# Kernel optimization log

Hardware: AMD Instinct MI355X
Metric: run time of the kernel (lower is better)

Reference implementation:

```python
import jax, jax.numpy as jnp
import numpy as np

EPS = 1e-5   # torch BatchNorm2d default eps
HEADS = 4


def conv1x1_bn(x, w, g, b, m, v):
    # 1x1 conv (no bias) == channel matmul, then inference-mode BatchNorm
    y = jnp.einsum('oc,bchw->bohw', w, x)
    s = g / jnp.sqrt(v + EPS)
    return y * s[None, :, None, None] + (b - m * s)[None, :, None, None]


def dwconv3x3_bn(x, w, g, b, m, v):
    # depthwise 3x3 conv, padding 1 (autopad), groups=C, then BatchNorm
    C = x.shape[1]
    y = jax.lax.conv_general_dilated(
        x, w, window_strides=(1, 1), padding=((1, 1), (1, 1)),
        dimension_numbers=('NCHW', 'OIHW', 'NCHW'), feature_group_count=C)
    s = g / jnp.sqrt(v + EPS)
    return y * s[None, :, None, None] + (b - m * s)[None, :, None, None]


def split_heads(x):
    b, c, h, w = x.shape
    hd = c // HEADS
    return x.reshape(b, HEADS, hd, h * w).transpose(0, 1, 3, 2)  # [b,heads,n,hd]


def merge_heads(x, h, w):
    b, heads, n, hd = x.shape
    return x.transpose(0, 1, 3, 2).reshape(b, heads * hd, h, w)


def setup_inputs() -> dict:
    key = jax.random.key(0)
    B, C, H, W = 4, 256, 48, 48
    ks = jax.random.split(key, 32)
    inp = {
        'q': jax.random.normal(ks[0], (B, C, H, W), jnp.float32),
        'k': jax.random.normal(ks[1], (B, C, H, W), jnp.float32),
        'v': jax.random.normal(ks[2], (B, C, H, W), jnp.float32),
    }
    i = 3
    for name in ['wq', 'wk', 'wv', 'proj']:
        inp[name + '_w'] = jax.random.normal(ks[i], (C, C), jnp.float32) * 0.02; i += 1
    inp['pe_w'] = jax.random.normal(ks[i], (C, 1, 3, 3), jnp.float32) * 0.1; i += 1
    for name in ['wq', 'wk', 'wv', 'pe', 'proj']:
        inp[name + '_g'] = jax.random.uniform(ks[i], (C,), jnp.float32, 0.5, 1.5); i += 1
        inp[name + '_b'] = jax.random.normal(ks[i], (C,), jnp.float32) * 0.1; i += 1
        inp[name + '_m'] = jax.random.normal(ks[i], (C,), jnp.float32) * 0.1; i += 1
        inp[name + '_v'] = jax.random.uniform(ks[i], (C,), jnp.float32, 0.5, 1.5); i += 1
    return inp


def reference(q, k, v,
              wq_w, wk_w, wv_w, proj_w, pe_w,
              wq_g, wq_b, wq_m, wq_v,
              wk_g, wk_b, wk_m, wk_v,
              wv_g, wv_b, wv_m, wv_v,
              pe_g, pe_b, pe_m, pe_v,
              proj_g, proj_b, proj_m, proj_v):
    H, W = q.shape[2], q.shape[3]
    qf = conv1x1_bn(q, wq_w, wq_g, wq_b, wq_m, wq_v)
    kf = conv1x1_bn(k, wk_w, wk_g, wk_b, wk_m, wk_v)
    vf = conv1x1_bn(v, wv_w, wv_g, wv_b, wv_m, wv_v)
    qh = split_heads(qf)  # [b,heads,n,hd]
    kh = split_heads(kf)
    vh = split_heads(vf)
    scale = qh.shape[-1] ** -0.5
    attn = jax.nn.softmax(jnp.einsum('bhnd,bhmd->bhnm', qh, kh) * scale, axis=-1)
    y = jnp.einsum('bhnm,bhmd->bhnd', attn, vh)
    y = merge_heads(y, H, W) + dwconv3x3_bn(merge_heads(qh, H, W), pe_w, pe_g, pe_b, pe_m, pe_v)
    return conv1x1_bn(y, proj_w, proj_g, proj_b, proj_m, proj_v)
```

## Files before the change

kernel.cpp:

```cpp
#include <hip/hip_runtime.h>
#include <math.h>

#define HEADS 4
#define HD    64
#define CCH   256
#define NB    4
#define HH    48
#define WW    48
#define NN    (HH*WW)
#define EPSBN 1e-5f
#define KSCL  0.18033688f
#define BCN   (NB*CCH*NN)
#define NSP   4

typedef unsigned short ushort_t;
typedef __attribute__((ext_vector_type(8))) short bfrag;
typedef __attribute__((ext_vector_type(4))) float f32x4;
typedef __attribute__((ext_vector_type(16))) float f32x16;

#define MFMA   __builtin_amdgcn_mfma_f32_16x16x32_bf16
#define MFMA32 __builtin_amdgcn_mfma_f32_32x32x16_bf16

static __device__ __forceinline__ ushort_t f2bf(float x) {
    unsigned int u = __float_as_uint(x);
    unsigned int r = (u + 0x7fffu + ((u >> 16) & 1u)) >> 16;
    return (ushort_t)r;
}
static __device__ __forceinline__ unsigned cvtpk(float lo, float hi) {
    unsigned r;
    asm("v_cvt_pk_bf16_f32 %0, %1, %2" : "=v"(r) : "v"(lo), "v"(hi));
    return r;
}
static __device__ __forceinline__ float fexp2(float x) {
    float r;
    asm("v_exp_f32 %0, %1" : "=v"(r) : "v"(x));
    return r;
}
static __device__ __forceinline__ float bflo(unsigned u) { return __uint_as_float(u << 16); }
static __device__ __forceinline__ float bfhi(unsigned u) { return __uint_as_float(u & 0xffff0000u); }

static __device__ __forceinline__ void gload16(const void* g, void* l) {
    __builtin_amdgcn_global_load_lds(
        (const __attribute__((address_space(1))) void*)g,
        (__attribute__((address_space(3))) void*)l, 16, 0, 0);
}

struct PrepWP {
    const float* W[4];
    const float* G[4]; const float* Bb[4]; const float* Mm[4]; const float* Vv[4];
    const float* pew; const float* peg; const float* peb; const float* pem; const float* pev;
    ushort_t* W4; float* bias4; ushort_t* pw2; float* pbias;
};
__global__ __launch_bounds__(256)
void prep_w(PrepWP P)
{
    const int blk = blockIdx.x, tid = threadIdx.x;
    if (blk == 128) {
        int c = tid;
        float s = P.peg[c] * rsqrtf(P.pev[c] + EPSBN);
        for (int tap = 0; tap < 9; ++tap)
            P.pw2[tap * CCH + c] = f2bf(P.pew[c * 9 + tap] * s);
        P.pbias[c] = P.peb[c] - P.pem[c] * s;
        return;
    }
    int g  = blk * 256 + tid;
    int cv = g >> 13;
    int o  = (g >> 5) & 255;
    int c8 = g & 31;
    float s  = P.G[cv][o] * rsqrtf(P.Vv[cv][o] + EPSBN);
    float s2 = (cv == 1) ? s * KSCL : s;
    const float* w = P.W[cv] + (size_t)o * CCH + c8 * 8;
    uint4 u;
    u.x = cvtpk(w[0]*s2, w[1]*s2); u.y = cvtpk(w[2]*s2, w[3]*s2);
    u.z = cvtpk(w[4]*s2, w[5]*s2); u.w = cvtpk(w[6]*s2, w[7]*s2);
    *(uint4*)&P.W4[((size_t)cv * CCH + o) * CCH + c8 * 8] = u;
    if (c8 == 0) {
        float bb = (P.Bb[cv][o] - P.Mm[cv][o] * s);
        P.bias4[cv * CCH + o] = (cv == 1) ? bb * KSCL : bb;
    }
}

template<int PROJ>
__global__ __launch_bounds__(512)
void conv_gemm(const float* __restrict__ qf, const float* __restrict__ kf,
               const float* __restrict__ vf, const ushort_t* __restrict__ T,
               const ushort_t* __restrict__ W4, const float* __restrict__ bias4,
               ushort_t* __restrict__ qnd, ushort_t* __restrict__ knd,
               ushort_t* __restrict__ vcn, float* __restrict__ outf)
{
    __shared__ ushort_t Ts[64][264];
    __shared__ ushort_t Ws[64][264];
    const int nt = blockIdx.x, ot = blockIdx.y, z = blockIdx.z;
    const int which = PROJ ? 3 : (z >> 2);
    const int b = z & 3;
    const int tid = threadIdx.x;
    const int n0 = nt * 64, o0 = ot * 64;
    const ushort_t* Wsrc = W4 + (size_t)which * CCH * CCH + (size_t)o0 * CCH;
    const float*    bias = bias4 + which * CCH;

    if (!PROJ) {
#pragma unroll
        for (int i = 0; i < 4; ++i) {
            int idx = tid + i * 512;
            int r = idx >> 5, c16 = idx & 31;
            *(uint4*)&Ws[r][c16 * 8] = *(const uint4*)&Wsrc[(size_t)r * CCH + c16 * 8];
        }
        const float* Xf = (which == 0) ? qf : (which == 1) ? kf : vf;
        const float* Xb = Xf + (size_t)b * CCH * NN + n0;
        const int n = tid & 63;
#pragma unroll
        for (int p = 0; p < 4; ++p) {
            int c0 = (tid >> 6) * 8 + p * 64;
            const float* src = Xb + (size_t)c0 * NN + n;
            float vv[8];
#pragma unroll
            for (int j = 0; j < 8; ++j) vv[j] = src[(size_t)j * NN];
            uint4 u;
            u.x = cvtpk(vv[0], vv[1]); u.y = cvtpk(vv[2], vv[3]);
            u.z = cvtpk(vv[4], vv[5]); u.w = cvtpk(vv[6], vv[7]);
            *(uint4*)&Ts[n][c0] = u;
        }
    } else {
        const ushort_t* Tsrc = T + ((size_t)b * NN + n0) * CCH;
#pragma unroll
        for (int i = 0; i < 4; ++i) {
            int idx = tid + i * 512;
            int r = idx >> 5, c16 = idx & 31;
            *(uint4*)&Ts[r][c16 * 8] = *(const uint4*)&Tsrc[(size_t)r * CCH + c16 * 8];
            *(uint4*)&Ws[r][c16 * 8] = *(const uint4*)&Wsrc[(size_t)r * CCH + c16 * 8];
        }
    }
    __syncthreads();
    const int wv = tid >> 6, lane = tid & 63, lr = lane & 15, lg = lane >> 4;
    const int qn = (wv >> 1) * 16, qo = (wv & 1) * 32;
    f32x4 acc[2];
    acc[0] = (f32x4){0.f, 0.f, 0.f, 0.f};
    acc[1] = (f32x4){0.f, 0.f, 0.f, 0.f};

    if (!PROJ && (z >> 2) < 2) {
#pragma unroll
        for (int k8 = 0; k8 < 8; ++k8) {
            const int kc = k8 * 32 + lg * 8;
            bfrag ta  = *(const bfrag*)&Ts[qn + lr][kc];
            bfrag wa0 = *(const bfrag*)&Ws[qo + lr][kc];
            bfrag wa1 = *(const bfrag*)&Ws[qo + 16 + lr][kc];
            acc[0] = MFMA(ta, wa0, acc[0], 0, 0, 0);
            acc[1] = MFMA(ta, wa1, acc[1], 0, 0, 0);
        }
    } else {
#pragma unroll
        for (int k8 = 0; k8 < 8; ++k8) {
            const int kc = k8 * 32 + lg * 8;
            bfrag ta  = *(const bfrag*)&Ts[qn + lr][kc];
            bfrag wa0 = *(const bfrag*)&Ws[qo + lr][kc];
            bfrag wa1 = *(const bfrag*)&Ws[qo + 16 + lr][kc];
            acc[0] = MFMA(wa0, ta, acc[0], 0, 0, 0);
            acc[1] = MFMA(wa1, ta, acc[1], 0, 0, 0);
        }
    }

    __syncthreads();
    if (!PROJ && which < 2) {
        ushort_t (*Ot)[72] = (ushort_t(*)[72])Ts;
        float bv[2] = { bias[o0 + qo + lr], bias[o0 + qo + 16 + lr] };
#pragma unroll
        for (int j = 0; j < 2; ++j)
#pragma unroll
            for (int r = 0; r < 4; ++r)
                Ot[qn + lg * 4 + r][qo + j * 16 + lr] = f2bf(acc[j][r] + bv[j]);
        __syncthreads();
        ushort_t* out = (which == 0) ? qnd : knd;
        {
            int r = tid >> 3, sg = tid & 7;
            *(uint4*)&out[(((size_t)b * HEADS + ot) * NN + n0 + r) * HD + sg * 8] =
                *(const uint4*)&Ot[r][sg * 8];
        }
    } else if (!PROJ) {
        ushort_t (*Ot)[72] = (ushort_t(*)[72])Ts;
#pragma unroll
        for (int j = 0; j < 2; ++j)
#pragma unroll
            for (int r = 0; r < 4; ++r) {
                float bv = bias[o0 + qo + j * 16 + lg * 4 + r];
                Ot[qo + j * 16 + lg * 4 + r][qn + lr] = f2bf(acc[j][r] + bv);
            }
        __syncthreads();
        {
            int r = tid >> 3, sg = tid & 7;
            *(uint4*)&vcn[((size_t)b * CCH + o0 + r) * NN + n0 + sg * 8] =
                *(const uint4*)&Ot[r][sg * 8];
        }
    } else {
        float (*Of)[68] = (float(*)[68])Ts;
#pragma unroll
        for (int j = 0; j < 2; ++j)
#pragma unroll
            for (int r = 0; r < 4; ++r) {
                float bv = bias[o0 + qo + j * 16 + lg * 4 + r];
                Of[qo + j * 16 + lg * 4 + r][qn + lr] = acc[j][r] + bv;
            }
        __syncthreads();
#pragma unroll
        for (int i = 0; i < 2; ++i) {
            int idx = tid + i * 512;
            int r = idx >> 4, c4 = idx & 15;
            *(float4*)&outf[((size_t)b * CCH + o0 + r) * NN + n0 + c4 * 4] =
                *(const float4*)&Of[r][c4 * 4];
        }
    }
}

__global__ __launch_bounds__(256, 4)
void attn_kernel(const ushort_t* __restrict__ Qnd,
                 const ushort_t* __restrict__ Knd,
                 const ushort_t* __restrict__ Vcn,
                 ushort_t* __restrict__ Op,
                 float* __restrict__ Larr)
{
    __shared__ __align__(16) char smem[32768];

    const int tid = threadIdx.x;
    const int lin0 = blockIdx.x + 18 * blockIdx.y + 288 * blockIdx.z;
    const int w    = (lin0 & 7) * 144 + (lin0 >> 3);
    const int qt = w % 18;
    const int bh = (w / 18) & 15;
    const int sp = w / 288;
    const int b = bh >> 2, h = bh & 3;
    const int lane = tid & 63, wv = tid >> 6;
    const int l31 = lane & 31, hi = lane >> 5, l7 = lane & 7;
    const int lrow = lane >> 3, lslot = (lane & 7) ^ lrow;
    const int n0 = qt * 128;
    const size_t ndb = (size_t)(b * HEADS + h) * NN * HD;
    const size_t cnb = ((size_t)b * CCH + h * HD) * NN;

    const char* kgp = (const char*)(Knd + ndb) + (size_t)(sp * 576 + wv * 16 + lrow) * 128 + lslot * 16;
    const char* vgp = (const char*)(Vcn + cnb + sp * 576) + (size_t)(wv * 16 + lrow) * (NN * 2) + lslot * 16;
    char* kls = smem + wv * 2048;
    char* vls = smem + 16384 + wv * 2048;

#define STAGE(buf, t) do { \
    const char* kp_ = kgp + (size_t)(t) * 8192; \
    const char* vp_ = vgp + (size_t)(t) * 128; \
    char* kd_ = kls + (buf) * 8192; \
    char* vd_ = vls + (buf) * 8192; \
    gload16(kp_,              kd_); \
    gload16(kp_ + 1024,       kd_ + 1024); \
    gload16(vp_,              vd_); \
    gload16(vp_ + 8 * (NN*2), vd_ + 1024); \
} while (0)

    bfrag qb[4];
    {
        const ushort_t* qbase = Qnd + ndb + (size_t)(n0 + wv * 32 + l31) * HD + hi * 8;
#pragma unroll
        for (int ds = 0; ds < 4; ++ds)
            qb[ds] = *(const bfrag*)&qbase[ds * 16];
    }

    f32x16 o[2];
#pragma unroll
    for (int db = 0; db < 2; ++db)
#pragma unroll
        for (int j = 0; j < 16; ++j) o[db][j] = 0.f;
    float lacc0 = 0.f, lacc1 = 0.f;

    STAGE(0, 0);

    for (int t = 0; t < 9; ++t) {
        const int cur = t & 1;
        asm volatile("s_waitcnt vmcnt(0)" ::: "memory");
        __builtin_amdgcn_s_barrier();
        if (t < 8) STAGE(cur ^ 1, t + 1);
        const char* Kb = smem + cur * 8192;
        const char* Vb = smem + 16384 + cur * 8192;

        bfrag pf[4];
#pragma unroll
        for (int kb = 0; kb < 2; ++kb) {
            f32x16 s;
#pragma unroll
            for (int j = 0; j < 16; ++j) s[j] = 0.f;
            __builtin_amdgcn_s_setprio(1);
#pragma unroll
            for (int ds = 0; ds < 4; ++ds) {
                const char* ka_p = Kb + (kb * 32 + l31) * 128 + (((2 * ds + hi) ^ l7) << 4);
                bfrag ka = *(const bfrag*)ka_p;
                s = MFMA32(ka, qb[ds], s, 0, 0, 0);
            }
            __builtin_amdgcn_s_setprio(0);
            float e[16];
#pragma unroll
            for (int j = 0; j < 16; ++j) e[j] = fexp2(s[j]);
#pragma unroll
            for (int j = 0; j < 8; ++j) { lacc0 += e[2 * j]; lacc1 += e[2 * j + 1]; }
            unsigned u[4][2];
#pragma unroll
            for (int g = 0; g < 4; ++g) {
                u[g][0] = cvtpk(e[4 * g + 0], e[4 * g + 1]);
                u[g][1] = cvtpk(e[4 * g + 2], e[4 * g + 3]);
            }
#pragma unroll
            for (int ks = 0; ks < 2; ++ks) {
                asm("v_permlane32_swap_b32 %0, %1" : "+v"(u[2*ks][0]), "+v"(u[2*ks+1][0]));
                asm("v_permlane32_swap_b32 %0, %1" : "+v"(u[2*ks][1]), "+v"(u[2*ks+1][1]));
                uint4 fw = { u[2*ks][0], u[2*ks][1], u[2*ks+1][0], u[2*ks+1][1] };
                pf[kb * 2 + ks] = *(const bfrag*)&fw;
            }
        }

        __builtin_amdgcn_s_setprio(1);
#pragma unroll
        for (int db = 0; db < 2; ++db)
#pragma unroll
            for (int ks = 0; ks < 4; ++ks) {
                const char* va_p = Vb + (db * 32 + l31) * 128 + (((2 * ks + hi) ^ l7) << 4);
                bfrag va = *(const bfrag*)va_p;
                o[db] = MFMA32(va, pf[ks], o[db], 0, 0, 0);
            }
        __builtin_amdgcn_s_setprio(0);
    }
#undef STAGE
    __builtin_amdgcn_s_barrier();

    float lacc = lacc0 + lacc1;
    lacc += __shfl_xor(lacc, 32);
    if (hi == 0)
        Larr[(size_t)(sp * 16 + bh) * NN + n0 + wv * 32 + l31] = lacc;

    unsigned (*Osb)[36] = (unsigned(*)[36])smem;
    {
        int row = wv * 32 + l31;
#pragma unroll
        for (int db = 0; db < 2; ++db)
#pragma unroll
            for (int g = 0; g < 4; ++g) {
                uint2 pk;
                pk.x = cvtpk(o[db][4 * g + 0], o[db][4 * g + 1]);
                pk.y = cvtpk(o[db][4 * g + 2], o[db][4 * g + 3]);
                *(uint2*)&Osb[row][16 * db + 4 * g + 2 * hi] = pk;
            }
    }
    __syncthreads();
    ushort_t* opb = Op + (size_t)sp * BCN + ((size_t)b * NN + n0) * CCH + h * HD;
    for (int idx = tid; idx < 1024; idx += 256) {
        int n = idx >> 3, s4 = idx & 7;
        *(uint4*)&opb[(size_t)n * CCH + s4 * 8] = *(const uint4*)&Osb[n][s4 * 4];
    }
}

__global__ __launch_bounds__(256)
void fuse_kernel(const ushort_t* __restrict__ Op, const float* __restrict__ Larr,
                 const ushort_t* __restrict__ Qnd,
                 const ushort_t* __restrict__ pw2, const float* __restrict__ pbias,
                 ushort_t* __restrict__ yt)
{
    const int tid = threadIdx.x;
    const int b  = blockIdx.x / 288;
    const int n0 = (blockIdx.x % 288) * 8;
    const int c8 = tid & 31, ns = tid >> 5;
    const int n  = n0 + ns;
    const int h  = c8 >> 3, c0 = c8 * 8;

    const ushort_t* o0p = Op + ((size_t)b * NN + n) * CCH + c0;
    float acc[8] = {0.f, 0.f, 0.f, 0.f, 0.f, 0.f, 0.f, 0.f};
#pragma unroll
    for (int s = 0; s < NSP; ++s) {
        uint4 u = *(const uint4*)&o0p[(size_t)s * BCN];
        acc[0] += bflo(u.x); acc[1] += bfhi(u.x);
        acc[2] += bflo(u.y); acc[3] += bfhi(u.y);
        acc[4] += bflo(u.z); acc[5] += bfhi(u.z);
        acc[6] += bflo(u.w); acc[7] += bfhi(u.w);
    }
    int mi = (b * HEADS + h) * NN + n;
    float ls = 0.f;
#pragma unroll
    for (int s = 0; s < NSP; ++s) ls += Larr[(size_t)s * 16 * NN + mi];
    float rinv = 1.0f / ls;
#pragma unroll
    for (int j = 0; j < 8; ++j) acc[j] *= rinv;

    const int x = n % WW, y = n / WW;
    const ushort_t* qb = Qnd + (size_t)(b * HEADS + h) * NN * HD + (c8 & 7) * 8;
#pragma unroll
    for (int ky = 0; ky < 3; ++ky) {
        int yy = y + ky - 1;
        if (yy < 0 || yy >= HH) continue;
#pragma unroll
        for (int kx = 0; kx < 3; ++kx) {
            int xx = x + kx - 1;
            if (xx < 0 || xx >= WW) continue;
            int np = yy * WW + xx;
            uint4 qv = *(const uint4*)&qb[(size_t)np * HD];
            uint4 w4 = *(const uint4*)&pw2[(ky * 3 + kx) * CCH + c0];
            acc[0] += bflo(qv.x) * bflo(w4.x); acc[1] += bfhi(qv.x) * bfhi(w4.x);
            acc[2] += bflo(qv.y) * bflo(w4.y); acc[3] += bfhi(qv.y) * bfhi(w4.y);
            acc[4] += bflo(qv.z) * bflo(w4.z); acc[5] += bfhi(qv.z) * bfhi(w4.z);
            acc[6] += bflo(qv.w) * bflo(w4.w); acc[7] += bfhi(qv.w) * bfhi(w4.w);
        }
    }
    float4 p0 = *(const float4*)&pbias[c0];
    float4 p1 = *(const float4*)&pbias[c0 + 4];
    acc[0] += p0.x; acc[1] += p0.y; acc[2] += p0.z; acc[3] += p0.w;
    acc[4] += p1.x; acc[5] += p1.y; acc[6] += p1.z; acc[7] += p1.w;
    uint4 u;
    u.x = cvtpk(acc[0], acc[1]); u.y = cvtpk(acc[2], acc[3]);
    u.z = cvtpk(acc[4], acc[5]); u.w = cvtpk(acc[6], acc[7]);
    *(uint4*)&yt[((size_t)b * NN + n) * CCH + c0] = u;
}

extern "C" void kernel_launch(void* const* d_in, const int* in_sizes, int n_in,
                              void* d_out, int out_size, void* d_ws, size_t ws_size,
                              hipStream_t stream) {
    const float* q = (const float*)d_in[0];
    const float* k = (const float*)d_in[1];
    const float* v = (const float*)d_in[2];

    char* ws = (char*)d_ws;
    ushort_t* qnd  = (ushort_t*)(ws + 0);
    ushort_t* knd  = (ushort_t*)(ws + 4718592);
    ushort_t* vcn  = (ushort_t*)(ws + 9437184);
    ushort_t* Op   = (ushort_t*)(ws + 14155776);
    ushort_t* yt   = (ushort_t*)(ws + 4718592);
    float*    Larr = (float*)   (ws + 33030144);
    ushort_t* W4   = (ushort_t*)(ws + 33619968);
    float*    bias4= (float*)   (ws + 34144256);
    ushort_t* pw2  = (ushort_t*)(ws + 34148352);
    float*    pbias= (float*)   (ws + 34152960);

    PrepWP P;
    P.W[0] = (const float*)d_in[3]; P.W[1] = (const float*)d_in[4];
    P.W[2] = (const float*)d_in[5]; P.W[3] = (const float*)d_in[6];
    P.G[0]  = (const float*)d_in[8];  P.Bb[0] = (const float*)d_in[9];
    P.Mm[0] = (const float*)d_in[10]; P.Vv[0] = (const float*)d_in[11];
    P.G[1]  = (const float*)d_in[12]; P.Bb[1] = (const float*)d_in[13];
    P.Mm[1] = (const float*)d_in[14]; P.Vv[1] = (const float*)d_in[15];
    P.G[2]  = (const float*)d_in[16]; P.Bb[2] = (const float*)d_in[17];
    P.Mm[2] = (const float*)d_in[18]; P.Vv[2] = (const float*)d_in[19];
    P.G[3]  = (const float*)d_in[24]; P.Bb[3] = (const float*)d_in[25];
    P.Mm[3] = (const float*)d_in[26]; P.Vv[3] = (const float*)d_in[27];
    P.pew = (const float*)d_in[7];
    P.peg = (const float*)d_in[20]; P.peb = (const float*)d_in[21];
    P.pem = (const float*)d_in[22]; P.pev = (const float*)d_in[23];
    P.W4 = W4; P.bias4 = bias4; P.pw2 = pw2; P.pbias = pbias;

    prep_w<<<129, 256, 0, stream>>>(P);

    conv_gemm<0><<<dim3(36, 4, 12), 512, 0, stream>>>(q, k, v, nullptr, W4, bias4,
                                                      qnd, knd, vcn, nullptr);

    attn_kernel<<<dim3(18, 16, NSP), 256, 0, stream>>>(qnd, knd, vcn, Op, Larr);

    fuse_kernel<<<1152, 256, 0, stream>>>(Op, Larr, qnd, pw2, pbias, yt);

    conv_gemm<1><<<dim3(36, 4, 4), 512, 0, stream>>>(nullptr, nullptr, nullptr, yt, W4, bias4,
                                                     nullptr, nullptr, nullptr, (float*)d_out);
}
```

Measured before the change: 75.10 us.

## Fold weight prep into GEMM/fuse kernels and raise attention KV splits to six

```diff
diff --git a/kernel.cpp b/kernel.cpp
--- a/kernel.cpp
+++ b/kernel.cpp
@@ -11,7 +11,6 @@
 #define EPSBN 1e-5f
 #define KSCL  0.18033688f
 #define BCN   (NB*CCH*NN)
-#define NSP   4
 
 typedef unsigned short ushort_t;
 typedef __attribute__((ext_vector_type(8))) short bfrag;
@@ -21,72 +20,42 @@
 #define MFMA   __builtin_amdgcn_mfma_f32_16x16x32_bf16
 #define MFMA32 __builtin_amdgcn_mfma_f32_32x32x16_bf16
 
+static __device__ __forceinline__ unsigned cvtpk(float lo, float hi) {
+    unsigned r;
+    asm("v_cvt_pk_bf16_f32 %0, %1, %2" : "=v"(r) : "v"(lo), "v"(hi));
+    return r;
+}
+static __device__ __forceinline__ float fexp2(float x) {
+    float r;
+    asm("v_exp_f32 %0, %1" : "=v"(r) : "v"(x));
+    return r;
+}
+static __device__ __forceinline__ float bflo(unsigned u) { return __uint_as_float(u << 16); }
+static __device__ __forceinline__ float bfhi(unsigned u) { return __uint_as_float(u & 0xffff0000u); }
+
+static __device__ __forceinline__ void gload16(const void* g, void* l) {
+    __builtin_amdgcn_global_load_lds(
+        (const __attribute__((address_space(1))) void*)g,
+        (__attribute__((address_space(3))) void*)l, 16, 0, 0);
+}
+
 static __device__ __forceinline__ ushort_t f2bf(float x) {
     unsigned int u = __float_as_uint(x);
     unsigned int r = (u + 0x7fffu + ((u >> 16) & 1u)) >> 16;
     return (ushort_t)r;
 }
-static __device__ __forceinline__ unsigned cvtpk(float lo, float hi) {
-    unsigned r;
-    asm("v_cvt_pk_bf16_f32 %0, %1, %2" : "=v"(r) : "v"(lo), "v"(hi));
-    return r;
-}
-static __device__ __forceinline__ float fexp2(float x) {
-    float r;
-    asm("v_exp_f32 %0, %1" : "=v"(r) : "v"(x));
-    return r;
-}
-static __device__ __forceinline__ float bflo(unsigned u) { return __uint_as_float(u << 16); }
-static __device__ __forceinline__ float bfhi(unsigned u) { return __uint_as_float(u & 0xffff0000u); }
-
-static __device__ __forceinline__ void gload16(const void* g, void* l) {
-    __builtin_amdgcn_global_load_lds(
-        (const __attribute__((address_space(1))) void*)g,
-        (__attribute__((address_space(3))) void*)l, 16, 0, 0);
-}
-
-struct PrepWP {
-    const float* W[4];
-    const float* G[4]; const float* Bb[4]; const float* Mm[4]; const float* Vv[4];
-    const float* pew; const float* peg; const float* peb; const float* pem; const float* pev;
-    ushort_t* W4; float* bias4; ushort_t* pw2; float* pbias;
+
+struct ConvP {
+    const float* X0; const float* X1; const float* X2;
+    const ushort_t* T;
+    const float* W[4]; const float* G[4]; const float* Bb[4];
+    const float* Mm[4]; const float* Vv[4];
+    ushort_t* qnd; ushort_t* knd; ushort_t* vcn; float* outf;
 };
-__global__ __launch_bounds__(256)
-void prep_w(PrepWP P)
-{
-    const int blk = blockIdx.x, tid = threadIdx.x;
-    if (blk == 128) {
-        int c = tid;
-        float s = P.peg[c] * rsqrtf(P.pev[c] + EPSBN);
-        for (int tap = 0; tap < 9; ++tap)
-            P.pw2[tap * CCH + c] = f2bf(P.pew[c * 9 + tap] * s);
-        P.pbias[c] = P.peb[c] - P.pem[c] * s;
-        return;
-    }
-    int g  = blk * 256 + tid;
-    int cv = g >> 13;
-    int o  = (g >> 5) & 255;
-    int c8 = g & 31;
-    float s  = P.G[cv][o] * rsqrtf(P.Vv[cv][o] + EPSBN);
-    float s2 = (cv == 1) ? s * KSCL : s;
-    const float* w = P.W[cv] + (size_t)o * CCH + c8 * 8;
-    uint4 u;
-    u.x = cvtpk(w[0]*s2, w[1]*s2); u.y = cvtpk(w[2]*s2, w[3]*s2);
-    u.z = cvtpk(w[4]*s2, w[5]*s2); u.w = cvtpk(w[6]*s2, w[7]*s2);
-    *(uint4*)&P.W4[((size_t)cv * CCH + o) * CCH + c8 * 8] = u;
-    if (c8 == 0) {
-        float bb = (P.Bb[cv][o] - P.Mm[cv][o] * s);
-        P.bias4[cv * CCH + o] = (cv == 1) ? bb * KSCL : bb;
-    }
-}
 
 template<int PROJ>
 __global__ __launch_bounds__(512)
-void conv_gemm(const float* __restrict__ qf, const float* __restrict__ kf,
-               const float* __restrict__ vf, const ushort_t* __restrict__ T,
-               const ushort_t* __restrict__ W4, const float* __restrict__ bias4,
-               ushort_t* __restrict__ qnd, ushort_t* __restrict__ knd,
-               ushort_t* __restrict__ vcn, float* __restrict__ outf)
+void conv_gemm(ConvP P)
 {
     __shared__ ushort_t Ts[64][264];
     __shared__ ushort_t Ws[64][264];
@@ -95,17 +64,29 @@
     const int b = z & 3;
     const int tid = threadIdx.x;
     const int n0 = nt * 64, o0 = ot * 64;
-    const ushort_t* Wsrc = W4 + (size_t)which * CCH * CCH + (size_t)o0 * CCH;
-    const float*    bias = bias4 + which * CCH;
-
+    const float* Wf  = P.W[which];
+    const float* Gf  = P.G[which];
+    const float* Bbf = P.Bb[which];
+    const float* Mmf = P.Mm[which];
+    const float* Vvf = P.Vv[which];
+    const float wmul = (which == 1) ? KSCL : 1.0f;
+
+#pragma unroll
+    for (int i = 0; i < 4; ++i) {
+        int idx = tid + i * 512;
+        int r = idx >> 5, c16 = idx & 31;
+        int o = o0 + r;
+        float s2 = Gf[o] * rsqrtf(Vvf[o] + EPSBN) * wmul;
+        const float* wp = Wf + (size_t)o * CCH + c16 * 8;
+        float4 wa = *(const float4*)&wp[0];
+        float4 wb = *(const float4*)&wp[4];
+        uint4 u;
+        u.x = cvtpk(wa.x * s2, wa.y * s2); u.y = cvtpk(wa.z * s2, wa.w * s2);
+        u.z = cvtpk(wb.x * s2, wb.y * s2); u.w = cvtpk(wb.z * s2, wb.w * s2);
+        *(uint4*)&Ws[r][c16 * 8] = u;
+    }
     if (!PROJ) {
-#pragma unroll
-        for (int i = 0; i < 4; ++i) {
-            int idx = tid + i * 512;
-            int r = idx >> 5, c16 = idx & 31;
-            *(uint4*)&Ws[r][c16 * 8] = *(const uint4*)&Wsrc[(size_t)r * CCH + c16 * 8];
-        }
-        const float* Xf = (which == 0) ? qf : (which == 1) ? kf : vf;
+        const float* Xf = (which == 0) ? P.X0 : (which == 1) ? P.X1 : P.X2;
         const float* Xb = Xf + (size_t)b * CCH * NN + n0;
         const int n = tid & 63;
 #pragma unroll
@@ -121,13 +102,12 @@
             *(uint4*)&Ts[n][c0] = u;
         }
     } else {
-        const ushort_t* Tsrc = T + ((size_t)b * NN + n0) * CCH;
+        const ushort_t* Tsrc = P.T + ((size_t)b * NN + n0) * CCH;
 #pragma unroll
         for (int i = 0; i < 4; ++i) {
             int idx = tid + i * 512;
             int r = idx >> 5, c16 = idx & 31;
             *(uint4*)&Ts[r][c16 * 8] = *(const uint4*)&Tsrc[(size_t)r * CCH + c16 * 8];
-            *(uint4*)&Ws[r][c16 * 8] = *(const uint4*)&Wsrc[(size_t)r * CCH + c16 * 8];
         }
     }
     __syncthreads();
@@ -137,7 +117,7 @@
     acc[0] = (f32x4){0.f, 0.f, 0.f, 0.f};
     acc[1] = (f32x4){0.f, 0.f, 0.f, 0.f};
 
-    if (!PROJ && (z >> 2) < 2) {
+    if (!PROJ && which < 2) {
 #pragma unroll
         for (int k8 = 0; k8 < 8; ++k8) {
             const int kc = k8 * 32 + lg * 8;
@@ -162,14 +142,20 @@
     __syncthreads();
     if (!PROJ && which < 2) {
         ushort_t (*Ot)[72] = (ushort_t(*)[72])Ts;
-        float bv[2] = { bias[o0 + qo + lr], bias[o0 + qo + 16 + lr] };
+        float bv[2];
+#pragma unroll
+        for (int j = 0; j < 2; ++j) {
+            int o = o0 + qo + j * 16 + lr;
+            float s = Gf[o] * rsqrtf(Vvf[o] + EPSBN);
+            bv[j] = (Bbf[o] - Mmf[o] * s) * wmul;
+        }
 #pragma unroll
         for (int j = 0; j < 2; ++j)
 #pragma unroll
             for (int r = 0; r < 4; ++r)
                 Ot[qn + lg * 4 + r][qo + j * 16 + lr] = f2bf(acc[j][r] + bv[j]);
         __syncthreads();
-        ushort_t* out = (which == 0) ? qnd : knd;
+        ushort_t* out = (which == 0) ? P.qnd : P.knd;
         {
             int r = tid >> 3, sg = tid & 7;
             *(uint4*)&out[(((size_t)b * HEADS + ot) * NN + n0 + r) * HD + sg * 8] =
@@ -181,13 +167,15 @@
         for (int j = 0; j < 2; ++j)
 #pragma unroll
             for (int r = 0; r < 4; ++r) {
-                float bv = bias[o0 + qo + j * 16 + lg * 4 + r];
+                int o = o0 + qo + j * 16 + lg * 4 + r;
+                float s = Gf[o] * rsqrtf(Vvf[o] + EPSBN);
+                float bv = Bbf[o] - Mmf[o] * s;
                 Ot[qo + j * 16 + lg * 4 + r][qn + lr] = f2bf(acc[j][r] + bv);
             }
         __syncthreads();
         {
             int r = tid >> 3, sg = tid & 7;
-            *(uint4*)&vcn[((size_t)b * CCH + o0 + r) * NN + n0 + sg * 8] =
+            *(uint4*)&P.vcn[((size_t)b * CCH + o0 + r) * NN + n0 + sg * 8] =
                 *(const uint4*)&Ot[r][sg * 8];
         }
     } else {
@@ -196,7 +184,9 @@
         for (int j = 0; j < 2; ++j)
 #pragma unroll
             for (int r = 0; r < 4; ++r) {
-                float bv = bias[o0 + qo + j * 16 + lg * 4 + r];
+                int o = o0 + qo + j * 16 + lg * 4 + r;
+                float s = Gf[o] * rsqrtf(Vvf[o] + EPSBN);
+                float bv = Bbf[o] - Mmf[o] * s;
                 Of[qo + j * 16 + lg * 4 + r][qn + lr] = acc[j][r] + bv;
             }
         __syncthreads();
@@ -204,12 +194,13 @@
         for (int i = 0; i < 2; ++i) {
             int idx = tid + i * 512;
             int r = idx >> 4, c4 = idx & 15;
-            *(float4*)&outf[((size_t)b * CCH + o0 + r) * NN + n0 + c4 * 4] =
+            *(float4*)&P.outf[((size_t)b * CCH + o0 + r) * NN + n0 + c4 * 4] =
                 *(const float4*)&Of[r][c4 * 4];
         }
     }
 }
 
+template<int NSPT>
 __global__ __launch_bounds__(256, 4)
 void attn_kernel(const ushort_t* __restrict__ Qnd,
                  const ushort_t* __restrict__ Knd,
@@ -217,11 +208,13 @@
                  ushort_t* __restrict__ Op,
                  float* __restrict__ Larr)
 {
+    constexpr int NT    = 36 / NSPT;
+    constexpr int CHUNK = 18 * 16 * NSPT / 8;
     __shared__ __align__(16) char smem[32768];
 
     const int tid = threadIdx.x;
     const int lin0 = blockIdx.x + 18 * blockIdx.y + 288 * blockIdx.z;
-    const int w    = (lin0 & 7) * 144 + (lin0 >> 3);
+    const int w    = (lin0 & 7) * CHUNK + (lin0 >> 3);
     const int qt = w % 18;
     const int bh = (w / 18) & 15;
     const int sp = w / 288;
@@ -233,8 +226,8 @@
     const size_t ndb = (size_t)(b * HEADS + h) * NN * HD;
     const size_t cnb = ((size_t)b * CCH + h * HD) * NN;
 
-    const char* kgp = (const char*)(Knd + ndb) + (size_t)(sp * 576 + wv * 16 + lrow) * 128 + lslot * 16;
-    const char* vgp = (const char*)(Vcn + cnb + sp * 576) + (size_t)(wv * 16 + lrow) * (NN * 2) + lslot * 16;
+    const char* kgp = (const char*)(Knd + ndb) + (size_t)(sp * (NT * 64) + wv * 16 + lrow) * 128 + lslot * 16;
+    const char* vgp = (const char*)(Vcn + cnb + sp * (NT * 64)) + (size_t)(wv * 16 + lrow) * (NN * 2) + lslot * 16;
     char* kls = smem + wv * 2048;
     char* vls = smem + 16384 + wv * 2048;
 
@@ -266,11 +259,11 @@
 
     STAGE(0, 0);
 
-    for (int t = 0; t < 9; ++t) {
+    for (int t = 0; t < NT; ++t) {
         const int cur = t & 1;
         asm volatile("s_waitcnt vmcnt(0)" ::: "memory");
         __builtin_amdgcn_s_barrier();
-        if (t < 8) STAGE(cur ^ 1, t + 1);
+        if (t < NT - 1) STAGE(cur ^ 1, t + 1);
         const char* Kb = smem + cur * 8192;
         const char* Vb = smem + 16384 + cur * 8192;
 
@@ -348,10 +341,13 @@
     }
 }
 
+template<int NSPT>
 __global__ __launch_bounds__(256)
 void fuse_kernel(const ushort_t* __restrict__ Op, const float* __restrict__ Larr,
                  const ushort_t* __restrict__ Qnd,
-                 const ushort_t* __restrict__ pw2, const float* __restrict__ pbias,
+                 const float* __restrict__ pew, const float* __restrict__ peg,
+                 const float* __restrict__ peb, const float* __restrict__ pem,
+                 const float* __restrict__ pev,
                  ushort_t* __restrict__ yt)
 {
     const int tid = threadIdx.x;
@@ -364,7 +360,7 @@
     const ushort_t* o0p = Op + ((size_t)b * NN + n) * CCH + c0;
     float acc[8] = {0.f, 0.f, 0.f, 0.f, 0.f, 0.f, 0.f, 0.f};
 #pragma unroll
-    for (int s = 0; s < NSP; ++s) {
+    for (int s = 0; s < NSPT; ++s) {
         uint4 u = *(const uint4*)&o0p[(size_t)s * BCN];
         acc[0] += bflo(u.x); acc[1] += bfhi(u.x);
         acc[2] += bflo(u.y); acc[3] += bfhi(u.y);
@@ -374,10 +370,19 @@
     int mi = (b * HEADS + h) * NN + n;
     float ls = 0.f;
 #pragma unroll
-    for (int s = 0; s < NSP; ++s) ls += Larr[(size_t)s * 16 * NN + mi];
+    for (int s = 0; s < NSPT; ++s) ls += Larr[(size_t)s * 16 * NN + mi];
     float rinv = 1.0f / ls;
 #pragma unroll
     for (int j = 0; j < 8; ++j) acc[j] *= rinv;
+
+    float ps_[8], pb_[8];
+#pragma unroll
+    for (int j = 0; j < 8; ++j) {
+        int c = c0 + j;
+        float s = peg[c] * rsqrtf(pev[c] + EPSBN);
+        ps_[j] = s;
+        pb_[j] = peb[c] - pem[c] * s;
+    }
 
     const int x = n % WW, y = n / WW;
     const ushort_t* qb = Qnd + (size_t)(b * HEADS + h) * NN * HD + (c8 & 7) * 8;
@@ -391,17 +396,19 @@
             if (xx < 0 || xx >= WW) continue;
             int np = yy * WW + xx;
             uint4 qv = *(const uint4*)&qb[(size_t)np * HD];
-            uint4 w4 = *(const uint4*)&pw2[(ky * 3 + kx) * CCH + c0];
-            acc[0] += bflo(qv.x) * bflo(w4.x); acc[1] += bfhi(qv.x) * bfhi(w4.x);
-            acc[2] += bflo(qv.y) * bflo(w4.y); acc[3] += bfhi(qv.y) * bfhi(w4.y);
-            acc[4] += bflo(qv.z) * bflo(w4.z); acc[5] += bfhi(qv.z) * bfhi(w4.z);
-            acc[6] += bflo(qv.w) * bflo(w4.w); acc[7] += bfhi(qv.w) * bfhi(w4.w);
-        }
-    }
-    float4 p0 = *(const float4*)&pbias[c0];
-    float4 p1 = *(const float4*)&pbias[c0 + 4];
-    acc[0] += p0.x; acc[1] += p0.y; acc[2] += p0.z; acc[3] += p0.w;
-    acc[4] += p1.x; acc[5] += p1.y; acc[6] += p1.z; acc[7] += p1.w;
+            const float* pwc = pew + (size_t)c0 * 9 + (ky * 3 + kx);
+            acc[0] += bflo(qv.x) * (pwc[0]  * ps_[0]);
+            acc[1] += bfhi(qv.x) * (pwc[9]  * ps_[1]);
+            acc[2] += bflo(qv.y) * (pwc[18] * ps_[2]);
+            acc[3] += bfhi(qv.y) * (pwc[27] * ps_[3]);
+            acc[4] += bflo(qv.z) * (pwc[36] * ps_[4]);
+            acc[5] += bfhi(qv.z) * (pwc[45] * ps_[5]);
+            acc[6] += bflo(qv.w) * (pwc[54] * ps_[6]);
+            acc[7] += bfhi(qv.w) * (pwc[63] * ps_[7]);
+        }
+    }
+#pragma unroll
+    for (int j = 0; j < 8; ++j) acc[j] += pb_[j];
     uint4 u;
     u.x = cvtpk(acc[0], acc[1]); u.y = cvtpk(acc[2], acc[3]);
     u.z = cvtpk(acc[4], acc[5]); u.w = cvtpk(acc[6], acc[7]);
@@ -411,23 +418,22 @@
 extern "C" void kernel_launch(void* const* d_in, const int* in_sizes, int n_in,
                               void* d_out, int out_size, void* d_ws, size_t ws_size,
                               hipStream_t stream) {
-    const float* q = (const float*)d_in[0];
-    const float* k = (const float*)d_in[1];
-    const float* v = (const float*)d_in[2];
-
     char* ws = (char*)d_ws;
-    ushort_t* qnd  = (ushort_t*)(ws + 0);
-    ushort_t* knd  = (ushort_t*)(ws + 4718592);
-    ushort_t* vcn  = (ushort_t*)(ws + 9437184);
-    ushort_t* Op   = (ushort_t*)(ws + 14155776);
-    ushort_t* yt   = (ushort_t*)(ws + 4718592);
-    float*    Larr = (float*)   (ws + 33030144);
-    ushort_t* W4   = (ushort_t*)(ws + 33619968);
-    float*    bias4= (float*)   (ws + 34144256);
-    ushort_t* pw2  = (ushort_t*)(ws + 34148352);
-    float*    pbias= (float*)   (ws + 34152960);
-
-    PrepWP P;
+    ushort_t* qnd = (ushort_t*)(ws + 0);
+    ushort_t* knd = (ushort_t*)(ws + 4718592);
+    ushort_t* vcn = (ushort_t*)(ws + 9437184);
+    ushort_t* Op  = (ushort_t*)(ws + 14155776);
+    ushort_t* yt  = (ushort_t*)(ws + 4718592);
+
+    const float* pew = (const float*)d_in[7];
+    const float* peg = (const float*)d_in[20], *peb = (const float*)d_in[21];
+    const float* pem = (const float*)d_in[22], *pev = (const float*)d_in[23];
+
+    ConvP P;
+    P.X0 = (const float*)d_in[0];
+    P.X1 = (const float*)d_in[1];
+    P.X2 = (const float*)d_in[2];
+    P.T  = yt;
     P.W[0] = (const float*)d_in[3]; P.W[1] = (const float*)d_in[4];
     P.W[2] = (const float*)d_in[5]; P.W[3] = (const float*)d_in[6];
     P.G[0]  = (const float*)d_in[8];  P.Bb[0] = (const float*)d_in[9];
@@ -438,20 +444,20 @@
     P.Mm[2] = (const float*)d_in[18]; P.Vv[2] = (const float*)d_in[19];
     P.G[3]  = (const float*)d_in[24]; P.Bb[3] = (const float*)d_in[25];
     P.Mm[3] = (const float*)d_in[26]; P.Vv[3] = (const float*)d_in[27];
-    P.pew = (const float*)d_in[7];
-    P.peg = (const float*)d_in[20]; P.peb = (const float*)d_in[21];
-    P.pem = (const float*)d_in[22]; P.pev = (const float*)d_in[23];
-    P.W4 = W4; P.bias4 = bias4; P.pw2 = pw2; P.pbias = pbias;
-
-    prep_w<<<129, 256, 0, stream>>>(P);
-
-    conv_gemm<0><<<dim3(36, 4, 12), 512, 0, stream>>>(q, k, v, nullptr, W4, bias4,
-                                                      qnd, knd, vcn, nullptr);
-
-    attn_kernel<<<dim3(18, 16, NSP), 256, 0, stream>>>(qnd, knd, vcn, Op, Larr);
-
-    fuse_kernel<<<1152, 256, 0, stream>>>(Op, Larr, qnd, pw2, pbias, yt);
-
-    conv_gemm<1><<<dim3(36, 4, 4), 512, 0, stream>>>(nullptr, nullptr, nullptr, yt, W4, bias4,
-                                                     nullptr, nullptr, nullptr, (float*)d_out);
-}
+    P.qnd = qnd; P.knd = knd; P.vcn = vcn; P.outf = (float*)d_out;
+
+    conv_gemm<0><<<dim3(36, 4, 12), 512, 0, stream>>>(P);
+
+    const size_t need6 = 14155776 + (size_t)6 * 4718592 + (size_t)6 * 16 * NN * 4;
+    if (ws_size >= need6) {
+        float* Larr = (float*)(ws + 14155776 + (size_t)6 * 4718592);
+        attn_kernel<6><<<dim3(18, 16, 6), 256, 0, stream>>>(qnd, knd, vcn, Op, Larr);
+        fuse_kernel<6><<<1152, 256, 0, stream>>>(Op, Larr, qnd, pew, peg, peb, pem, pev, yt);
+    } else {
+        float* Larr = (float*)(ws + 14155776 + (size_t)4 * 4718592);
+        attn_kernel<4><<<dim3(18, 16, 4), 256, 0, stream>>>(qnd, knd, vcn, Op, Larr);
+        fuse_kernel<4><<<1152, 256, 0, stream>>>(Op, Larr, qnd, pew, peg, peb, pem, pev, yt);
+    }
+
+    conv_gemm<1><<<dim3(36, 4, 4), 512, 0, stream>>>(P);
+}
```

New measurement: 111.7 us. 1.49x slower.
